# Kernel optimization log

Measured on AMD Instinct MI355X. Metric: run time of the kernel, lower is better.

Reference implementation:

```python
import jax, jax.numpy as jnp
import numpy as np

D_MODEL = 1024
N_HEADS = 16
D_K = D_MODEL // N_HEADS
B, T = 2, 2048


def setup_inputs() -> dict:
    key = jax.random.key(0)
    ks = jax.random.split(key, 12)
    s = 0.02
    return {
        "q": jax.random.normal(ks[0], (B, T, D_MODEL), jnp.float32),
        "k": jax.random.normal(ks[1], (B, T, D_MODEL), jnp.float32),
        "v": jax.random.normal(ks[2], (B, T, D_MODEL), jnp.float32),
        "Wq": jax.random.normal(ks[3], (D_MODEL, D_MODEL), jnp.float32) * s,
        "bq": jnp.zeros((D_MODEL,), jnp.float32),
        "Wk": jax.random.normal(ks[4], (D_MODEL, D_MODEL), jnp.float32) * s,
        "bk": jnp.zeros((D_MODEL,), jnp.float32),
        "Wv": jax.random.normal(ks[5], (D_MODEL, D_MODEL), jnp.float32) * s,
        "bv": jnp.zeros((D_MODEL,), jnp.float32),
        "Wo": jax.random.normal(ks[6], (D_MODEL, D_MODEL), jnp.float32) * s,
        "bo": jnp.zeros((D_MODEL,), jnp.float32),
        "mask": jnp.ones((B, T), jnp.int32),
        "causal": 1,
    }


def reference(q, k, v, Wq, bq, Wk, bk, Wv, bv, Wo, bo, mask, causal):
    Bq, Tq, D = q.shape
    Tk = k.shape[1]
    # projections (torch Linear: x @ W.T + b), split heads -> [B, H, T, d_k]
    qh = (q @ Wq.T + bq).reshape(Bq, Tq, N_HEADS, D_K).transpose(0, 2, 1, 3)
    kh = (k @ Wk.T + bk).reshape(Bq, Tk, N_HEADS, D_K).transpose(0, 2, 1, 3)
    vh = (v @ Wv.T + bv).reshape(Bq, Tk, N_HEADS, D_K).transpose(0, 2, 1, 3)
    scores = jnp.einsum("bhqd,bhkd->bhqk", qh, kh) / jnp.sqrt(jnp.float32(D_K))
    neg_inf = jnp.float32(-jnp.inf)
    if mask is not None:
        scores = jnp.where(mask[:, None, None, :] == 0, neg_inf, scores)
    if causal:
        causal_mask = jnp.tril(jnp.ones((Tq, Tq), jnp.float32))
        scores = jnp.where(causal_mask == 0, neg_inf, scores)
    attn = jax.nn.softmax(scores, axis=-1)
    out = jnp.einsum("bhqk,bhkd->bhqd", attn, vh)
    out = out.transpose(0, 2, 1, 3).reshape(Bq, Tq, D)
    return out @ Wo.T + bo
```

## Files before the change

### kernel.cpp

```cpp
#include <hip/hip_runtime.h>
#include <cstdint>
#include <cstddef>


typedef __bf16 bf16x8 __attribute__((ext_vector_type(8)));
typedef float f32x4 __attribute__((ext_vector_type(4)));

#define MFMA(a, b, c) __builtin_amdgcn_mfma_f32_16x16x32_bf16((a), (b), (c), 0, 0, 0)

static constexpr int D_MODEL = 1024;
static constexpr int T_ = 2048;
static constexpr int M_TOK = 4096;

__device__ __forceinline__ unsigned short f32_to_bf16(float f) {
    union { float f; uint32_t u; } v; v.f = f;
    uint32_t u = v.u;
    uint32_t r = u + 0x7fffu + ((u >> 16) & 1u);
    return (unsigned short)(r >> 16);
}
__device__ __forceinline__ unsigned pk2(float a, float b) {
    union { __bf16 h[2]; unsigned u; } z;
    z.h[0] = (__bf16)a; z.h[1] = (__bf16)b;
    return z.u;
}

typedef __attribute__((address_space(1))) void* as1_ptr;
typedef __attribute__((address_space(3))) void* as3_ptr;
__device__ __forceinline__ void gload_lds16(const void* g, void* l) {
    __builtin_amdgcn_global_load_lds((as1_ptr)(void*)g, (as3_ptr)l, 16, 0, 0);
}

__device__ __forceinline__ int keyperm(int k) {
    return (k & 32) | ((k & 12) << 1) | ((k & 16) >> 2) | (k & 3);
}

__global__ __launch_bounds__(256) void cvt_all(
    const float* __restrict__ q, const float* __restrict__ k,
    const float* __restrict__ v, const float* __restrict__ wq,
    const float* __restrict__ wk, const float* __restrict__ wv,
    const float* __restrict__ wo, ushort4* __restrict__ dst) {
    int i = blockIdx.x * blockDim.x + threadIdx.x;
    constexpr int R = 1 << 20;
    const float* s;
    int idx;
    if (i < 3 * R) {
        s = (i < R) ? q : (i < 2 * R) ? k : v;
        idx = i & (R - 1);
    } else {
        int j = i - 3 * R;
        int w = j >> 18;
        s = (w == 0) ? wq : (w == 1) ? wk : (w == 2) ? wv : wo;
        idx = j & ((1 << 18) - 1);
    }
    float4 f = ((const float4*)s)[idx];
    ushort4 o;
    o.x = (unsigned short)f32_to_bf16(f.x); o.y = (unsigned short)f32_to_bf16(f.y);
    o.z = (unsigned short)f32_to_bf16(f.z); o.w = (unsigned short)f32_to_bf16(f.w);
    dst[i] = o;
}

template<int MODE, int NT16>
__device__ __forceinline__ void gemm_body(
    const unsigned short* __restrict__ A, const unsigned short* __restrict__ W,
    const float* __restrict__ bias, void* __restrict__ outp,
    unsigned short* As, unsigned short* Ws, int bx, int by, float oscale)
{
    constexpr bool SWAP = (MODE != 2);
    constexpr int BKE = 32;
    constexpr int ASZ = 128 * BKE;
    constexpr int WSZ = NT16 * 32 * BKE;
    constexpr int AL = ASZ / (256 * 8);
    constexpr int WL = WSZ / (256 * 8);
    constexpr int NKS = D_MODEL / BKE;
    const int tid = threadIdx.x;
    const int lane = tid & 63, wave = tid >> 6;
    const int wm = wave >> 1, wn = wave & 1;
    const int r16 = lane & 15, kg = lane >> 4;
    const int m_blk = by * 128, n_blk = bx * (NT16 * 32);

    const unsigned short* Ap[AL]; unsigned short* Albase[AL];
    #pragma unroll
    for (int j = 0; j < AL; ++j) {
        int si = j * 256 + tid;
        int row = si >> 2, p = si & 3, g = p ^ ((row >> 1) & 3);
        Ap[j] = A + (size_t)(m_blk + row) * D_MODEL + g * 8;
        Albase[j] = As + (j * 256 + wave * 64) * 8;
    }
    const unsigned short* Wp[WL]; unsigned short* Wlbase[WL];
    #pragma unroll
    for (int j = 0; j < WL; ++j) {
        int si = j * 256 + tid;
        int row = si >> 2, p = si & 3, g = p ^ ((row >> 1) & 3);
        Wp[j] = W + (size_t)(n_blk + row) * D_MODEL + g * 8;
        Wlbase[j] = Ws + (j * 256 + wave * 64) * 8;
    }

    int aoff[4], woff[NT16];
    #pragma unroll
    for (int mt = 0; mt < 4; ++mt) {
        int row = wm * 64 + mt * 16 + r16;
        aoff[mt] = row * BKE + ((kg ^ ((row >> 1) & 3)) * 8);
    }
    #pragma unroll
    for (int nt = 0; nt < NT16; ++nt) {
        int row = wn * (NT16 * 16) + nt * 16 + r16;
        woff[nt] = row * BKE + ((kg ^ ((row >> 1) & 3)) * 8);
    }

    f32x4 acc[4][NT16];
    #pragma unroll
    for (int mt = 0; mt < 4; ++mt)
        #pragma unroll
        for (int nt = 0; nt < NT16; ++nt) acc[mt][nt] = (f32x4){0, 0, 0, 0};

    auto stage = [&](int bb, int k0) {
        #pragma unroll
        for (int j = 0; j < AL; ++j)
            gload_lds16(Ap[j] + k0, Albase[j] + bb * ASZ);
        #pragma unroll
        for (int j = 0; j < WL; ++j)
            gload_lds16(Wp[j] + k0, Wlbase[j] + bb * WSZ);
    };

    stage(0, 0);
    stage(1, BKE);
    int cb = 0;
    for (int ks = 0; ks < NKS; ++ks) {
        if (ks + 1 < NKS) asm volatile("s_waitcnt vmcnt(4)" ::: "memory");
        else              asm volatile("s_waitcnt vmcnt(0)" ::: "memory");
        __builtin_amdgcn_s_barrier();
        __builtin_amdgcn_sched_barrier(0);
        if (ks + 2 < NKS) {
            int sb = cb + 2; if (sb >= 3) sb -= 3;
            stage(sb, (ks + 2) * BKE);
        }
        const unsigned short* Asb = As + cb * ASZ;
        const unsigned short* Wsb = Ws + cb * WSZ;
        bf16x8 af[4], wf[NT16];
        #pragma unroll
        for (int mt = 0; mt < 4; ++mt)
            af[mt] = *(const bf16x8*)(Asb + aoff[mt]);
        #pragma unroll
        for (int nt = 0; nt < NT16; ++nt)
            wf[nt] = *(const bf16x8*)(Wsb + woff[nt]);
        #pragma unroll
        for (int mt = 0; mt < 4; ++mt)
            #pragma unroll
            for (int nt = 0; nt < NT16; ++nt)
                acc[mt][nt] = SWAP ? MFMA(wf[nt], af[mt], acc[mt][nt])
                                   : MFMA(af[mt], wf[nt], acc[mt][nt]);
        cb = (cb == 2) ? 0 : cb + 1;
    }

    if (MODE == 2) {
        #pragma unroll
        for (int nt = 0; nt < NT16; ++nt) {
            int n = n_blk + wn * (NT16 * 16) + nt * 16 + r16;
            float bn = bias[n];
            int hh = n >> 6, dki = n & 63;
            #pragma unroll
            for (int mt = 0; mt < 4; ++mt) {
                int m0 = m_blk + wm * 64 + mt * 16 + kg * 4;
                int mp = (m0 & ~63) | keyperm(m0 & 63);
                int bb = mp >> 11, ti = mp & 2047;
                ushort4 pk;
                pk.x = f32_to_bf16((acc[mt][nt][0] + bn) * oscale);
                pk.y = f32_to_bf16((acc[mt][nt][1] + bn) * oscale);
                pk.z = f32_to_bf16((acc[mt][nt][2] + bn) * oscale);
                pk.w = f32_to_bf16((acc[mt][nt][3] + bn) * oscale);
                *(ushort4*)((unsigned short*)outp +
                    ((size_t)(bb * 16 + hh) * 64 + dki) * 2048 + ti) = pk;
            }
        }
    } else {
        #pragma unroll
        for (int nt = 0; nt < NT16; ++nt) {
            int n0 = n_blk + wn * (NT16 * 16) + nt * 16 + kg * 4;
            float4 bn4 = *(const float4*)(bias + n0);
            #pragma unroll
            for (int mt = 0; mt < 4; ++mt) {
                int m = m_blk + wm * 64 + mt * 16 + r16;
                if (MODE == 3) {
                    float4 st;
                    st.x = (acc[mt][nt][0] + bn4.x) * oscale;
                    st.y = (acc[mt][nt][1] + bn4.y) * oscale;
                    st.z = (acc[mt][nt][2] + bn4.z) * oscale;
                    st.w = (acc[mt][nt][3] + bn4.w) * oscale;
                    *(float4*)((float*)outp + (size_t)m * D_MODEL + n0) = st;
                } else {
                    ushort4 pk;
                    pk.x = f32_to_bf16((acc[mt][nt][0] + bn4.x) * oscale);
                    pk.y = f32_to_bf16((acc[mt][nt][1] + bn4.y) * oscale);
                    pk.z = f32_to_bf16((acc[mt][nt][2] + bn4.z) * oscale);
                    pk.w = f32_to_bf16((acc[mt][nt][3] + bn4.w) * oscale);
                    *(ushort4*)((unsigned short*)outp + (size_t)m * D_MODEL + n0) = pk;
                }
            }
        }
    }
}

__global__ __launch_bounds__(256) void gemm_qkv(
    const unsigned short* __restrict__ qb, const unsigned short* __restrict__ kb,
    const unsigned short* __restrict__ vb, const unsigned short* __restrict__ Wqb,
    const unsigned short* __restrict__ Wkb, const unsigned short* __restrict__ Wvb,
    const float* __restrict__ bq, const float* __restrict__ bk, const float* __restrict__ bv,
    unsigned short* __restrict__ Qhp, unsigned short* __restrict__ Khp,
    unsigned short* __restrict__ Vtp)
{
    __shared__ __align__(16) unsigned short As[3 * 128 * 32];
    __shared__ __align__(16) unsigned short Ws[3 * 128 * 32];
    int flat = blockIdx.x + (blockIdx.y << 3) + (blockIdx.z << 8);
    int w = (flat & 7) * 96 + (flat >> 3);
    int bx = w & 7, by = (w >> 3) & 31, z = w >> 8;
    const unsigned short* A = (z == 0) ? qb : (z == 1) ? kb : vb;
    const unsigned short* W = (z == 0) ? Wqb : (z == 1) ? Wkb : Wvb;
    const float* bias = (z == 0) ? bq : (z == 1) ? bk : bv;
    float osc = (z == 0) ? 0.18033688011112042f : 1.0f;
    if (z < 2)
        gemm_body<0, 4>(A, W, bias, (z == 0) ? (void*)Qhp : (void*)Khp, As, Ws,
                        bx, by, osc);
    else
        gemm_body<2, 4>(A, W, bias, (void*)Vtp, As, Ws, bx, by, 1.0f);
}

__global__ __launch_bounds__(256) void gemm_out(
    const unsigned short* __restrict__ ab, const unsigned short* __restrict__ Wob,
    const float* __restrict__ bo, float* __restrict__ outp)
{
    __shared__ __align__(16) unsigned short As[3 * 128 * 32];
    __shared__ __align__(16) unsigned short Ws[3 * 128 * 32];
    int flat = blockIdx.x + (blockIdx.y << 3);
    int w = (flat & 7) * 32 + (flat >> 3);
    int bx = w & 7, by = w >> 3;
    gemm_body<3, 4>(ab, Wob, bo, (void*)outp, As, Ws, bx, by, 1.0f);
}

__global__ __launch_bounds__(256) void attn_fwd(
    const unsigned short* __restrict__ Qh, const unsigned short* __restrict__ Kh,
    const unsigned short* __restrict__ Vt, const int* __restrict__ mask,
    const int* __restrict__ causal_p, unsigned short* __restrict__ attnout)
{
    __shared__ __align__(16) unsigned short Ks[3][64 * 64];
    __shared__ __align__(16) unsigned short Vs[3][64 * 64];
    __shared__ unsigned long long kmS[32];

    const int tid = threadIdx.x;
    const int lane = tid & 63, wave = tid >> 6;
    const int bh = blockIdx.x;
    const int y = blockIdx.y, y0 = y & 7, j4 = y >> 3;
    const int qc = (j4 == 0) ? (31 - y0) : (j4 == 1) ? (16 + y0)
                 : (j4 == 2) ? (15 - y0) : y0;
    const int b = bh >> 4, h = bh & 15;
    const int causal = *causal_p;
    const int r16 = lane & 15, kg = lane >> 4;

    const int q0 = qc * 64 + wave * 16;

    const unsigned short* Qb = Qh + (size_t)b * T_ * D_MODEL + h * 64;
    const unsigned short* Kb = Kh + (size_t)b * T_ * D_MODEL + h * 64;
    const unsigned short* Vb = Vt + (size_t)bh * 64 * T_;
    const int* mb = mask + b * T_;

    for (int t = wave; t < 32; t += 4) {
        unsigned long long m = __ballot(mb[t * 64 + lane] != 0);
        if (lane == 0) kmS[t] = m;
    }

    bf16x8 qf0 = *(const bf16x8*)(Qb + (size_t)(q0 + r16) * D_MODEL + kg * 8);
    bf16x8 qf1 = *(const bf16x8*)(Qb + (size_t)(q0 + r16) * D_MODEL + 32 + kg * 8);

    union { unsigned u[4]; bf16x8 v; } onef;
    onef.u[0] = onef.u[1] = onef.u[2] = onef.u[3] = 0x3f803f80u;

    f32x4 lacc = (f32x4){0, 0, 0, 0};
    f32x4 o[4];
    #pragma unroll
    for (int f = 0; f < 4; ++f) o[f] = (f32x4){0, 0, 0, 0};
    const int lim = wave * 16 + r16;

    const int nT = causal ? (qc + 1) : 32;

    const unsigned short* Kp[2]; const unsigned short* Vp[2];
    char* Kl[2]; char* Vl[2];
    #pragma unroll
    for (int j = 0; j < 2; ++j) {
        int si = j * 256 + tid;
        int row = si >> 3, cg = (si & 7) ^ (row & 7);
        Kp[j] = Kb + (size_t)row * D_MODEL + cg * 8;
        Vp[j] = Vb + (size_t)row * T_ + cg * 8;
        Kl[j] = (char*)Ks[0] + (j * 256 + wave * 64) * 16;
        Vl[j] = (char*)Vs[0] + (j * 256 + wave * 64) * 16;
    }
    auto stage = [&](int buf, int t) {
        #pragma unroll
        for (int j = 0; j < 2; ++j) {
            gload_lds16(Kp[j] + ((size_t)t << 16), Kl[j] + buf * 8192);
            gload_lds16(Vp[j] + (t << 6),          Vl[j] + buf * 8192);
        }
    };

#define TILE_ITER(CB)                                                          \
    {                                                                          \
        if (t + 1 < nT) asm volatile("s_waitcnt vmcnt(4)" ::: "memory");       \
        else            asm volatile("s_waitcnt vmcnt(0)" ::: "memory");       \
        __builtin_amdgcn_s_barrier();                                          \
        __builtin_amdgcn_sched_barrier(0);                                     \
        if (t + 2 < nT) stage((CB + 2) % 3, t + 2);                            \
        const unsigned short* Kst = Ks[CB];                                    \
        const unsigned short* Vst = Vs[CB];                                    \
        const bool diag = causal && (t == qc);                                 \
        unsigned long long km = kmS[t];                                        \
        f32x4 s[4];                                                            \
        __builtin_amdgcn_s_setprio(1);                                         \
        _Pragma("unroll")                                                      \
        for (int c = 0; c < 4; ++c) {                                          \
            int key = c * 16 + r16;                                            \
            bf16x8 kf0 = *(const bf16x8*)(Kst + key * 64 + ((kg ^ (key & 7)) * 8));       \
            bf16x8 kf1 = *(const bf16x8*)(Kst + key * 64 + (((4 + kg) ^ (key & 7)) * 8)); \
            f32x4 z = (f32x4){0, 0, 0, 0};                                     \
            z = MFMA(kf0, qf0, z);                                             \
            z = MFMA(kf1, qf1, z);                                             \
            s[c] = z;                                                          \
        }                                                                      \
        __builtin_amdgcn_s_setprio(0);                                         \
        float pv[4][4];                                                        \
        if (!diag && km == ~0ull) {                                            \
            _Pragma("unroll")                                                  \
            for (int c = 0; c < 4; ++c)                                        \
                _Pragma("unroll")                                              \
                for (int r = 0; r < 4; ++r)                                    \
                    pv[c][r] = __builtin_amdgcn_exp2f(s[c][r]);                \
        } else {                                                               \
            _Pragma("unroll")                                                  \
            for (int c = 0; c < 4; ++c) {                                      \
                unsigned mc = (unsigned)(km >> (c * 16));                      \
                _Pragma("unroll")                                              \
                for (int r = 0; r < 4; ++r) {                                  \
                    int kbit = kg * 4 + r;                                     \
                    bool ok = ((mc >> kbit) & 1) && (!diag || (c * 16 + kbit <= lim)); \
                    pv[c][r] = ok ? __builtin_amdgcn_exp2f(s[c][r]) : 0.f;     \
                }                                                              \
            }                                                                  \
        }                                                                      \
        union pk_t { unsigned u[4]; bf16x8 v; };                               \
        pk_t pa[2];                                                            \
        _Pragma("unroll")                                                      \
        for (int c = 0; c < 4; ++c) {                                          \
            int half = (c & 1) * 2;                                            \
            pa[c >> 1].u[half]     = pk2(pv[c][0], pv[c][1]);                  \
            pa[c >> 1].u[half + 1] = pk2(pv[c][2], pv[c][3]);                  \
        }                                                                      \
        __builtin_amdgcn_s_setprio(1);                                         \
        lacc = MFMA(pa[0].v, onef.v, lacc);                                    \
        lacc = MFMA(pa[1].v, onef.v, lacc);                                    \
        _Pragma("unroll")                                                      \
        for (int f = 0; f < 4; ++f) {                                          \
            int row = f * 16 + r16;                                            \
            int rx = row & 7;                                                  \
            _Pragma("unroll")                                                  \
            for (int cp = 0; cp < 2; ++cp) {                                   \
                int g = cp * 4 + kg;                                           \
                bf16x8 vf = *(const bf16x8*)(Vst + row * 64 + ((g ^ rx) * 8)); \
                o[f] = MFMA(pa[cp].v, vf, o[f]);                               \
            }                                                                  \
        }                                                                      \
        __builtin_amdgcn_s_setprio(0);                                         \
    }

    stage(0, 0);
    stage(1, 1);
    __syncthreads();
    int t = 0;
    while (t + 3 <= nT) {
        TILE_ITER(0); ++t;
        TILE_ITER(1); ++t;
        TILE_ITER(2); ++t;
    }
    if (t < nT) { TILE_ITER(0); ++t; }
    if (t < nT) { TILE_ITER(1); ++t; }
#undef TILE_ITER

    #pragma unroll
    for (int r = 0; r < 4; ++r) {
        float iv = (lacc[r] > 0.f) ? 1.0f / lacc[r] : 0.f;
        size_t base = ((size_t)(b * T_ + q0 + kg * 4 + r)) * D_MODEL + h * 64;
        #pragma unroll
        for (int f = 0; f < 4; ++f)
            attnout[base + f * 16 + r16] = f32_to_bf16(o[f][r] * iv);
    }
}

extern "C" void kernel_launch(void* const* d_in, const int* in_sizes, int n_in,
                              void* d_out, int out_size, void* d_ws, size_t ws_size,
                              hipStream_t stream) {
    const float* q  = (const float*)d_in[0];
    const float* k  = (const float*)d_in[1];
    const float* v  = (const float*)d_in[2];
    const float* Wq = (const float*)d_in[3];
    const float* bq = (const float*)d_in[4];
    const float* Wk = (const float*)d_in[5];
    const float* bk = (const float*)d_in[6];
    const float* Wv = (const float*)d_in[7];
    const float* bv = (const float*)d_in[8];
    const float* Wo = (const float*)d_in[9];
    const float* bo = (const float*)d_in[10];
    const int* mask   = (const int*)d_in[11];
    const int* causal = (const int*)d_in[12];

    const size_t SZ_TOK = (size_t)M_TOK * D_MODEL;
    const size_t SZ_W   = (size_t)D_MODEL * D_MODEL;

    unsigned short* qb  = (unsigned short*)d_ws;
    unsigned short* kb  = qb  + SZ_TOK;
    unsigned short* vb  = kb  + SZ_TOK;
    unsigned short* Wqb = vb  + SZ_TOK;
    unsigned short* Wkb = Wqb + SZ_W;
    unsigned short* Wvb = Wkb + SZ_W;
    unsigned short* Wob = Wvb + SZ_W;
    unsigned short* Qhp = Wob + SZ_W;
    unsigned short* Khp = Qhp + SZ_TOK;
    unsigned short* Vtp = Khp + SZ_TOK;
    unsigned short* ab  = Vtp + SZ_TOK;

    cvt_all<<<16384, 256, 0, stream>>>(q, k, v, Wq, Wk, Wv, Wo, (ushort4*)qb);

    gemm_qkv<<<dim3(D_MODEL / 128, M_TOK / 128, 3), 256, 0, stream>>>(
        qb, kb, vb, Wqb, Wkb, Wvb, bq, bk, bv, Qhp, Khp, Vtp);

    attn_fwd<<<dim3(32, 32), 256, 0, stream>>>(Qhp, Khp, Vtp, mask, causal, ab);

    gemm_out<<<dim3(D_MODEL / 128, M_TOK / 128), 256, 0, stream>>>(ab, Wob, bo,
                                                                   (float*)d_out);
}
```

Before: 213.5 us.

## Process two 64-row query tiles per attention block to reuse K/V tiles

Each attention block now handles 128 query rows (two 16-row sub-tiles per wave) instead of 64, halving the grid along the query dimension. Every K/V tile staged into LDS is reused for two query sub-tiles, which halves K/V global traffic and LDS fragment reads per query row. In exchange, register pressure roughly doubles (two sets of accumulators and scores), occupancy may drop, the grid has half as many blocks, and the causal mask now spans two diagonal tiles per block, wasting some work on the first sub-tile's final key tile.

```diff
diff --git a/kernel.cpp b/kernel.cpp
--- a/kernel.cpp
+++ b/kernel.cpp
@@ -248,14 +248,13 @@
     const int tid = threadIdx.x;
     const int lane = tid & 63, wave = tid >> 6;
     const int bh = blockIdx.x;
-    const int y = blockIdx.y, y0 = y & 7, j4 = y >> 3;
-    const int qc = (j4 == 0) ? (31 - y0) : (j4 == 1) ? (16 + y0)
-                 : (j4 == 2) ? (15 - y0) : y0;
+    const int y = blockIdx.y, y0 = y & 7;
+    const int c2 = (y >> 3) == 0 ? (15 - y0) : y0;
     const int b = bh >> 4, h = bh & 15;
     const int causal = *causal_p;
     const int r16 = lane & 15, kg = lane >> 4;
 
-    const int q0 = qc * 64 + wave * 16;
+    const int q0 = c2 * 128 + wave * 16;
 
     const unsigned short* Qb = Qh + (size_t)b * T_ * D_MODEL + h * 64;
     const unsigned short* Kb = Kh + (size_t)b * T_ * D_MODEL + h * 64;
@@ -267,19 +266,21 @@
         if (lane == 0) kmS[t] = m;
     }
 
-    bf16x8 qf0 = *(const bf16x8*)(Qb + (size_t)(q0 + r16) * D_MODEL + kg * 8);
-    bf16x8 qf1 = *(const bf16x8*)(Qb + (size_t)(q0 + r16) * D_MODEL + 32 + kg * 8);
+    bf16x8 qa0 = *(const bf16x8*)(Qb + (size_t)(q0 + r16) * D_MODEL + kg * 8);
+    bf16x8 qa1 = *(const bf16x8*)(Qb + (size_t)(q0 + r16) * D_MODEL + 32 + kg * 8);
+    bf16x8 qb0 = *(const bf16x8*)(Qb + (size_t)(q0 + 64 + r16) * D_MODEL + kg * 8);
+    bf16x8 qb1 = *(const bf16x8*)(Qb + (size_t)(q0 + 64 + r16) * D_MODEL + 32 + kg * 8);
 
     union { unsigned u[4]; bf16x8 v; } onef;
     onef.u[0] = onef.u[1] = onef.u[2] = onef.u[3] = 0x3f803f80u;
 
-    f32x4 lacc = (f32x4){0, 0, 0, 0};
-    f32x4 o[4];
-    #pragma unroll
-    for (int f = 0; f < 4; ++f) o[f] = (f32x4){0, 0, 0, 0};
+    f32x4 lac0 = (f32x4){0, 0, 0, 0}, lac1 = (f32x4){0, 0, 0, 0};
+    f32x4 o0[4], o1[4];
+    #pragma unroll
+    for (int f = 0; f < 4; ++f) { o0[f] = (f32x4){0, 0, 0, 0}; o1[f] = (f32x4){0, 0, 0, 0}; }
     const int lim = wave * 16 + r16;
 
-    const int nT = causal ? (qc + 1) : 32;
+    const int nT = causal ? (2 * c2 + 2) : 32;
 
     const unsigned short* Kp[2]; const unsigned short* Vp[2];
     char* Kl[2]; char* Vl[2];
@@ -309,51 +310,61 @@
         if (t + 2 < nT) stage((CB + 2) % 3, t + 2);                            \
         const unsigned short* Kst = Ks[CB];                                    \
         const unsigned short* Vst = Vs[CB];                                    \
-        const bool diag = causal && (t == qc);                                 \
         unsigned long long km = kmS[t];                                        \
-        f32x4 s[4];                                                            \
+        f32x4 s0[4], s1[4];                                                    \
         __builtin_amdgcn_s_setprio(1);                                         \
         _Pragma("unroll")                                                      \
         for (int c = 0; c < 4; ++c) {                                          \
             int key = c * 16 + r16;                                            \
             bf16x8 kf0 = *(const bf16x8*)(Kst + key * 64 + ((kg ^ (key & 7)) * 8));       \
             bf16x8 kf1 = *(const bf16x8*)(Kst + key * 64 + (((4 + kg) ^ (key & 7)) * 8)); \
-            f32x4 z = (f32x4){0, 0, 0, 0};                                     \
-            z = MFMA(kf0, qf0, z);                                             \
-            z = MFMA(kf1, qf1, z);                                             \
-            s[c] = z;                                                          \
+            f32x4 z0 = (f32x4){0, 0, 0, 0};                                    \
+            z0 = MFMA(kf0, qa0, z0); z0 = MFMA(kf1, qa1, z0); s0[c] = z0;      \
+            f32x4 z1 = (f32x4){0, 0, 0, 0};                                    \
+            z1 = MFMA(kf0, qb0, z1); z1 = MFMA(kf1, qb1, z1); s1[c] = z1;      \
         }                                                                      \
         __builtin_amdgcn_s_setprio(0);                                         \
-        float pv[4][4];                                                        \
-        if (!diag && km == ~0ull) {                                            \
+        float pv0[4][4], pv1[4][4];                                            \
+        bool fastp = (km == ~0ull) && (!causal || t < 2 * c2);                 \
+        if (fastp) {                                                           \
             _Pragma("unroll")                                                  \
             for (int c = 0; c < 4; ++c)                                        \
                 _Pragma("unroll")                                              \
-                for (int r = 0; r < 4; ++r)                                    \
-                    pv[c][r] = __builtin_amdgcn_exp2f(s[c][r]);                \
+                for (int r = 0; r < 4; ++r) {                                  \
+                    pv0[c][r] = __builtin_amdgcn_exp2f(s0[c][r]);              \
+                    pv1[c][r] = __builtin_amdgcn_exp2f(s1[c][r]);              \
+                }                                                              \
         } else {                                                               \
+            int lv0 = (!causal || t < 2 * c2) ? 63 : ((t == 2 * c2) ? lim : -1); \
+            int lv1 = (!causal || t <= 2 * c2) ? 63 : lim;                     \
             _Pragma("unroll")                                                  \
             for (int c = 0; c < 4; ++c) {                                      \
                 unsigned mc = (unsigned)(km >> (c * 16));                      \
                 _Pragma("unroll")                                              \
                 for (int r = 0; r < 4; ++r) {                                  \
                     int kbit = kg * 4 + r;                                     \
-                    bool ok = ((mc >> kbit) & 1) && (!diag || (c * 16 + kbit <= lim)); \
-                    pv[c][r] = ok ? __builtin_amdgcn_exp2f(s[c][r]) : 0.f;     \
+                    bool mk = (mc >> kbit) & 1;                                \
+                    int kl = c * 16 + kbit;                                    \
+                    pv0[c][r] = (mk && kl <= lv0) ? __builtin_amdgcn_exp2f(s0[c][r]) : 0.f; \
+                    pv1[c][r] = (mk && kl <= lv1) ? __builtin_amdgcn_exp2f(s1[c][r]) : 0.f; \
                 }                                                              \
             }                                                                  \
         }                                                                      \
         union pk_t { unsigned u[4]; bf16x8 v; };                               \
-        pk_t pa[2];                                                            \
+        pk_t pa0[2], pa1[2];                                                   \
         _Pragma("unroll")                                                      \
         for (int c = 0; c < 4; ++c) {                                          \
             int half = (c & 1) * 2;                                            \
-            pa[c >> 1].u[half]     = pk2(pv[c][0], pv[c][1]);                  \
-            pa[c >> 1].u[half + 1] = pk2(pv[c][2], pv[c][3]);                  \
+            pa0[c >> 1].u[half]     = pk2(pv0[c][0], pv0[c][1]);               \
+            pa0[c >> 1].u[half + 1] = pk2(pv0[c][2], pv0[c][3]);               \
+            pa1[c >> 1].u[half]     = pk2(pv1[c][0], pv1[c][1]);               \
+            pa1[c >> 1].u[half + 1] = pk2(pv1[c][2], pv1[c][3]);               \
         }                                                                      \
         __builtin_amdgcn_s_setprio(1);                                         \
-        lacc = MFMA(pa[0].v, onef.v, lacc);                                    \
-        lacc = MFMA(pa[1].v, onef.v, lacc);                                    \
+        lac0 = MFMA(pa0[0].v, onef.v, lac0);                                   \
+        lac0 = MFMA(pa0[1].v, onef.v, lac0);                                   \
+        lac1 = MFMA(pa1[0].v, onef.v, lac1);                                   \
+        lac1 = MFMA(pa1[1].v, onef.v, lac1);                                   \
         _Pragma("unroll")                                                      \
         for (int f = 0; f < 4; ++f) {                                          \
             int row = f * 16 + r16;                                            \
@@ -362,7 +373,8 @@
             for (int cp = 0; cp < 2; ++cp) {                                   \
                 int g = cp * 4 + kg;                                           \
                 bf16x8 vf = *(const bf16x8*)(Vst + row * 64 + ((g ^ rx) * 8)); \
-                o[f] = MFMA(pa[cp].v, vf, o[f]);                               \
+                o0[f] = MFMA(pa0[cp].v, vf, o0[f]);                            \
+                o1[f] = MFMA(pa1[cp].v, vf, o1[f]);                            \
             }                                                                  \
         }                                                                      \
         __builtin_amdgcn_s_setprio(0);                                         \
@@ -383,11 +395,15 @@
 
     #pragma unroll
     for (int r = 0; r < 4; ++r) {
-        float iv = (lacc[r] > 0.f) ? 1.0f / lacc[r] : 0.f;
-        size_t base = ((size_t)(b * T_ + q0 + kg * 4 + r)) * D_MODEL + h * 64;
-        #pragma unroll
-        for (int f = 0; f < 4; ++f)
-            attnout[base + f * 16 + r16] = f32_to_bf16(o[f][r] * iv);
+        float iv0 = (lac0[r] > 0.f) ? 1.0f / lac0[r] : 0.f;
+        float iv1 = (lac1[r] > 0.f) ? 1.0f / lac1[r] : 0.f;
+        size_t base0 = ((size_t)(b * T_ + q0 + kg * 4 + r)) * D_MODEL + h * 64;
+        size_t base1 = ((size_t)(b * T_ + q0 + 64 + kg * 4 + r)) * D_MODEL + h * 64;
+        #pragma unroll
+        for (int f = 0; f < 4; ++f) {
+            attnout[base0 + f * 16 + r16] = f32_to_bf16(o0[f][r] * iv0);
+            attnout[base1 + f * 16 + r16] = f32_to_bf16(o1[f][r] * iv1);
+        }
     }
 }
 
@@ -428,7 +444,7 @@
     gemm_qkv<<<dim3(D_MODEL / 128, M_TOK / 128, 3), 256, 0, stream>>>(
         qb, kb, vb, Wqb, Wkb, Wvb, bq, bk, bv, Qhp, Khp, Vtp);
 
-    attn_fwd<<<dim3(32, 32), 256, 0, stream>>>(Qhp, Khp, Vtp, mask, causal, ab);
+    attn_fwd<<<dim3(32, 16), 256, 0, stream>>>(Qhp, Khp, Vtp, mask, causal, ab);
 
     gemm_out<<<dim3(D_MODEL / 128, M_TOK / 128), 256, 0, stream>>>(ab, Wob, bo,
                                                                    (float*)d_out);
```

After: 220.4 us. +3.2%, slower.

## Double-buffer V tiles and keep key-mask flags in a register bitmask

Applied to the files above, without the earlier changes.

The attention kernel drops V staging from three LDS buffers to two, prefetching V one tile ahead while K stays triple-buffered two tiles ahead. The wait count and the unrolled loop are adjusted for the mixed 3/2 buffer rotation. The shared key-mask array is replaced by a per-thread bitmask of fully unmasked tiles, and the ballot is recomputed only for partial or diagonal tiles. The goal is lower LDS use per block, so more blocks fit per CU, at the cost of a shallower V prefetch that may expose load latency.

```diff
diff --git a/kernel.cpp b/kernel.cpp
--- a/kernel.cpp
+++ b/kernel.cpp
@@ -242,8 +242,7 @@
     const int* __restrict__ causal_p, unsigned short* __restrict__ attnout)
 {
     __shared__ __align__(16) unsigned short Ks[3][64 * 64];
-    __shared__ __align__(16) unsigned short Vs[3][64 * 64];
-    __shared__ unsigned long long kmS[32];
+    __shared__ __align__(16) unsigned short Vs[2][64 * 64];
 
     const int tid = threadIdx.x;
     const int lane = tid & 63, wave = tid >> 6;
@@ -262,9 +261,12 @@
     const unsigned short* Vb = Vt + (size_t)bh * 64 * T_;
     const int* mb = mask + b * T_;
 
-    for (int t = wave; t < 32; t += 4) {
-        unsigned long long m = __ballot(mb[t * 64 + lane] != 0);
-        if (lane == 0) kmS[t] = m;
+    const int nT = causal ? (qc + 1) : 32;
+
+    unsigned allm = 0;
+    for (int tt = 0; tt < nT; ++tt) {
+        unsigned long long m = __ballot(mb[tt * 64 + lane] != 0);
+        if (m == ~0ull) allm |= (1u << tt);
     }
 
     bf16x8 qf0 = *(const bf16x8*)(Qb + (size_t)(q0 + r16) * D_MODEL + kg * 8);
@@ -278,8 +280,6 @@
     #pragma unroll
     for (int f = 0; f < 4; ++f) o[f] = (f32x4){0, 0, 0, 0};
     const int lim = wave * 16 + r16;
-
-    const int nT = causal ? (qc + 1) : 32;
 
     const unsigned short* Kp[2]; const unsigned short* Vp[2];
     char* Kl[2]; char* Vl[2];
@@ -292,25 +292,28 @@
         Kl[j] = (char*)Ks[0] + (j * 256 + wave * 64) * 16;
         Vl[j] = (char*)Vs[0] + (j * 256 + wave * 64) * 16;
     }
-    auto stage = [&](int buf, int t) {
-        #pragma unroll
-        for (int j = 0; j < 2; ++j) {
+    auto stageK = [&](int buf, int t) {
+        #pragma unroll
+        for (int j = 0; j < 2; ++j)
             gload_lds16(Kp[j] + ((size_t)t << 16), Kl[j] + buf * 8192);
-            gload_lds16(Vp[j] + (t << 6),          Vl[j] + buf * 8192);
-        }
     };
-
-#define TILE_ITER(CB)                                                          \
+    auto stageV = [&](int buf, int t) {
+        #pragma unroll
+        for (int j = 0; j < 2; ++j)
+            gload_lds16(Vp[j] + (t << 6), Vl[j] + buf * 8192);
+    };
+
+#define TILE_ITER(KB, VB)                                                      \
     {                                                                          \
-        if (t + 1 < nT) asm volatile("s_waitcnt vmcnt(4)" ::: "memory");       \
+        if (t + 1 < nT) asm volatile("s_waitcnt vmcnt(2)" ::: "memory");       \
         else            asm volatile("s_waitcnt vmcnt(0)" ::: "memory");       \
         __builtin_amdgcn_s_barrier();                                          \
         __builtin_amdgcn_sched_barrier(0);                                     \
-        if (t + 2 < nT) stage((CB + 2) % 3, t + 2);                            \
-        const unsigned short* Kst = Ks[CB];                                    \
-        const unsigned short* Vst = Vs[CB];                                    \
+        if (t + 1 < nT) stageV(((VB) + 1) & 1, t + 1);            \
+        if (t + 2 < nT) stageK(((KB) + 2) % 3, t + 2);            \
+        const unsigned short* Kst = Ks[KB];                                    \
+        const unsigned short* Vst = Vs[VB];                                    \
         const bool diag = causal && (t == qc);                                 \
-        unsigned long long km = kmS[t];                                        \
         f32x4 s[4];                                                            \
         __builtin_amdgcn_s_setprio(1);                                         \
         _Pragma("unroll")                                                      \
@@ -325,13 +328,14 @@
         }                                                                      \
         __builtin_amdgcn_s_setprio(0);                                         \
         float pv[4][4];                                                        \
-        if (!diag && km == ~0ull) {                                            \
+        if (!diag && ((allm >> t) & 1)) {                                      \
             _Pragma("unroll")                                                  \
             for (int c = 0; c < 4; ++c)                                        \
                 _Pragma("unroll")                                              \
                 for (int r = 0; r < 4; ++r)                                    \
                     pv[c][r] = __builtin_amdgcn_exp2f(s[c][r]);                \
         } else {                                                               \
+            unsigned long long km = __ballot(mb[t * 64 + lane] != 0);          \
             _Pragma("unroll")                                                  \
             for (int c = 0; c < 4; ++c) {                                      \
                 unsigned mc = (unsigned)(km >> (c * 16));                      \
@@ -368,17 +372,26 @@
         __builtin_amdgcn_s_setprio(0);                                         \
     }
 
-    stage(0, 0);
-    stage(1, 1);
+    stageK(0, 0);
+    stageV(0, 0);
+    stageK(1, 1);
     __syncthreads();
     int t = 0;
-    while (t + 3 <= nT) {
-        TILE_ITER(0); ++t;
-        TILE_ITER(1); ++t;
-        TILE_ITER(2); ++t;
-    }
-    if (t < nT) { TILE_ITER(0); ++t; }
-    if (t < nT) { TILE_ITER(1); ++t; }
+    while (t + 6 <= nT) {
+        TILE_ITER(0, 0); ++t;
+        TILE_ITER(1, 1); ++t;
+        TILE_ITER(2, 0); ++t;
+        TILE_ITER(0, 1); ++t;
+        TILE_ITER(1, 0); ++t;
+        TILE_ITER(2, 1); ++t;
+    }
+    {
+        int kb = 0;
+        for (; t < nT; ++t) {
+            TILE_ITER(kb, t & 1);
+            kb = (kb == 2) ? 0 : kb + 1;
+        }
+    }
 #undef TILE_ITER
 
     #pragma unroll
```

Measured after the change: 216.0 us. No clear change (+1.1%).
